# Optimization experiments

Hardware: AMD Instinct MI355X
Metric: run time of the kernel (lower is better)

Reference implementation:

```python
import jax, jax.numpy as jnp
import numpy as np
from jax.ops import segment_sum, segment_max

N, E, B, F, CG = 20000, 320000, 64, 256, 92
NL, NP = 4, 3  # transformer conv layers, ppe layers
SQ = float(np.sqrt(F))


def setup_inputs() -> dict:
    ks = iter(jax.random.split(jax.random.key(0), 64))
    p = lambda *s: jax.random.normal(next(ks), s, jnp.float32) * 0.02
    return {
        "x": jax.random.uniform(next(ks), (N, CG), jnp.float32, 0.0, 10.0),
        "edge_index": jax.random.randint(next(ks), (2, E), 0, N, dtype=jnp.int32),
        "edge_attr": jax.random.normal(next(ks), (E, 3), jnp.float32),
        "batch": jnp.sort(jax.random.randint(next(ks), (N,), 0, B, dtype=jnp.int32)),
        "num_osda": jax.random.uniform(next(ks), (B,), jnp.float32, 1.0, 4.0),
        "ae_W1": p(F, CG), "ae_b1": p(F), "ae_W2": p(F, F), "ae_b2": p(F),
        "ee_W": p(F, F), "ee_b": p(F),
        "pe_W": p(F, CG), "pe_b": p(F),
        "Wq": p(NL, F, F), "bq": p(NL, F), "Wk": p(NL, F, F), "bk": p(NL, F),
        "Wv": p(NL, F, F), "bv": p(NL, F), "We": p(NL, F, F), "be": p(NL, F),
        "Ws": p(NL, F, F), "bs": p(NL, F),
        "pW1": p(NP, 2 * F, F), "pb1": p(NP, 2 * F),
        "pW2": p(NP, F, F), "pb2": p(NP, F),
        "pW3": p(NP, F, F), "pb3": p(NP, F),
        "pg": jnp.ones((NP, F), jnp.float32), "pbeta": jnp.zeros((NP, F), jnp.float32),
        "fc_W": p(F, F), "fc_b": p(F), "out_W": p(1, F), "out_b": p(1),
    }


def _forward(x, edge_index, edge_attr, batch, num_osda, ae_W1, ae_b1, ae_W2, ae_b2,
             ee_W, ee_b, pe_W, pe_b, Wq, bq, Wk, bk, Wv, bv, We, be, Ws, bs,
             pW1, pb1, pW2, pb2, pW3, pb3, pg, pbeta, fc_W, fc_b, out_W, out_b):
    src, dst = edge_index[0], edge_index[1]
    # atom embedding on floor(x): Lin -> SiLU -> Lin
    h = jax.nn.silu(jnp.floor(x) @ ae_W1.T + ae_b1) @ ae_W2.T + ae_b2   # [N,F]
    # ppe embedding on frac(x)*1000
    ppe = ((x - jnp.trunc(x)) * 1000.0) @ pe_W.T + pe_b                 # [N,F]
    # edge embedding: scalar -1/||edge_attr|| -> RBF(vmin=-6,vmax=0,bins=256) -> Lin -> SiLU
    d = -1.0 / jnp.linalg.norm(edge_attr, axis=1)                       # [E]
    centers = jnp.linspace(-6.0, 0.0, F)
    gamma = 1.0 / (6.0 / (F - 1))  # 1/mean(diff(centers))
    rbf = jnp.exp(-gamma * (d[:, None] - centers) ** 2)                 # [E,F]
    ef = jax.nn.silu(rbf @ ee_W.T + ee_b)                               # [E,F]

    def conv(h, i):
        # graph transformer conv (heads=1): softmax over incoming edges per node
        q = h @ Wq[i].T + bq[i]
        k = h @ Wk[i].T + bk[i]
        v = h @ Wv[i].T + bv[i]
        e = ef @ We[i].T + be[i]
        kj = k[src] + e                                                 # [E,F]
        vj = v[src] + e                                                 # [E,F]
        s = jnp.sum(q[dst] * kj, axis=-1) / SQ                          # [E]
        m = segment_max(s, dst, num_segments=N)
        ex = jnp.exp(s - m[dst])
        den = segment_sum(ex, dst, num_segments=N)
        alpha = ex / den[dst]
        agg = segment_sum(alpha[:, None] * vj, dst, num_segments=N)     # [N,F]
        return agg + h @ Ws[i].T + bs[i]                                # root/skip

    def ppe_conv(h, adj, i):
        adj = adj + h
        bn = adj * pg[i] + pbeta[i]  # eval-mode BatchNorm1d (running mean 0, var 1)
        a2 = bn @ pW1[i].T + pb1[i]                                     # [N,2F]
        x1 = a2[:, :F] @ pW2[i].T + pb2[i]
        x2 = jax.nn.gelu(a2[:, F:], approximate=False)  # dropout = identity (eval)
        return (x1 * x2) @ pW3[i].T + pb3[i] + h, adj

    for i in range(NP):
        h = conv(h, i)
        h, ppe = ppe_conv(h, ppe, i)
    h = conv(h, NL - 1)

    # scatter-mean pooling over graphs
    cnt = jnp.maximum(segment_sum(jnp.ones((N,), h.dtype), batch, num_segments=B), 1.0)
    tot = segment_sum(h, batch, num_segments=B) / cnt[:, None]          # [B,F]
    crystal = tot + jax.nn.silu(tot @ fc_W.T + fc_b)
    out = crystal @ out_W.T + out_b                                     # [B,1]
    return jnp.squeeze(out, -1) / num_osda                             # [B]


def reference(x, edge_index, edge_attr, batch, num_osda, ae_W1, ae_b1, ae_W2, ae_b2,
              ee_W, ee_b, pe_W, pe_b, Wq, bq, Wk, bk, Wv, bv, We, be, Ws, bs,
              pW1, pb1, pW2, pb2, pW3, pb3, pg, pbeta, fc_W, fc_b, out_W, out_b):
    return _forward(x, edge_index, edge_attr, batch, num_osda, ae_W1, ae_b1, ae_W2, ae_b2,
                    ee_W, ee_b, pe_W, pe_b, Wq, bq, Wk, bk, Wv, bv, We, be, Ws, bs,
                    pW1, pb1, pW2, pb2, pW3, pb3, pg, pbeta, fc_W, fc_b, out_W, out_b)
```

## Files before the change

### kernel.cpp

```cpp
#include <hip/hip_runtime.h>
#include <cstdint>
#include <cstddef>


#define DEVFN static __device__ __forceinline__

DEVFN float siluf(float x) { return x / (1.f + expf(-x)); }

DEVFN unsigned short f2bf(float x) {
    union { float f; unsigned u; } v; v.f = x;
    return (unsigned short)((v.u + 0x7FFFu + ((v.u >> 16) & 1u)) >> 16);
}
DEVFN float bf2f(unsigned short h) {
    union { unsigned u; float f; } v; v.u = ((unsigned)h) << 16;
    return v.f;
}

typedef __attribute__((ext_vector_type(8))) short bf16x8;
typedef __attribute__((ext_vector_type(4))) float f32x4;

#define O_F32    0
#define O_F32P   1
#define O_PPE1   4
#define O_PLANES 5

template <int ACT, int OMODE>
__launch_bounds__(256) __global__
void gemm_spp(const short* __restrict__ Ahi, const short* __restrict__ Alo, int lda,
              const short* __restrict__ Whi, const short* __restrict__ Wlo, int ldw,
              const float* __restrict__ bias,
              const float* __restrict__ res, int ldr,
              float* __restrict__ C, short* __restrict__ P1, short* __restrict__ P2,
              int ldc, int M, int OUT, int K)
{
    constexpr int LDP = 40;
    __shared__ short AsH[128 * LDP];
    __shared__ short AsL[128 * LDP];
    __shared__ short WsH[128 * LDP];
    __shared__ short WsL[128 * LDP];
    const int tid = threadIdx.x;
    const int bm = blockIdx.x * 128;
    const int bn = blockIdx.y * 128;
    const int w = tid >> 6, lane = tid & 63;
    const int wm = (w >> 1) * 64, wn = (w & 1) * 64;
    const int lr = lane & 15, lc = lane >> 4;

    f32x4 acc[4][4];
#pragma unroll
    for (int i = 0; i < 4; ++i)
#pragma unroll
        for (int j = 0; j < 4; ++j) acc[i][j] = (f32x4){0.f, 0.f, 0.f, 0.f};

    const int srow = tid & 127;
    const int scol0 = (tid >> 7) * 16;

    for (int k0 = 0; k0 < K; k0 += 32) {
        {
            int gm = bm + srow;
            if (gm < M) {
                const short* ah = Ahi + (size_t)gm * lda + k0 + scol0;
                const short* al = Alo + (size_t)gm * lda + k0 + scol0;
                *reinterpret_cast<bf16x8*>(&AsH[srow * LDP + scol0])     = *reinterpret_cast<const bf16x8*>(ah);
                *reinterpret_cast<bf16x8*>(&AsH[srow * LDP + scol0 + 8]) = *reinterpret_cast<const bf16x8*>(ah + 8);
                *reinterpret_cast<bf16x8*>(&AsL[srow * LDP + scol0])     = *reinterpret_cast<const bf16x8*>(al);
                *reinterpret_cast<bf16x8*>(&AsL[srow * LDP + scol0 + 8]) = *reinterpret_cast<const bf16x8*>(al + 8);
            } else {
                bf16x8 z = {0, 0, 0, 0, 0, 0, 0, 0};
                *reinterpret_cast<bf16x8*>(&AsH[srow * LDP + scol0])     = z;
                *reinterpret_cast<bf16x8*>(&AsH[srow * LDP + scol0 + 8]) = z;
                *reinterpret_cast<bf16x8*>(&AsL[srow * LDP + scol0])     = z;
                *reinterpret_cast<bf16x8*>(&AsL[srow * LDP + scol0 + 8]) = z;
            }
        }
        {
            int go = bn + srow;
            if (go < OUT) {
                const short* wh = Whi + (size_t)go * ldw + k0 + scol0;
                const short* wl = Wlo + (size_t)go * ldw + k0 + scol0;
                *reinterpret_cast<bf16x8*>(&WsH[srow * LDP + scol0])     = *reinterpret_cast<const bf16x8*>(wh);
                *reinterpret_cast<bf16x8*>(&WsH[srow * LDP + scol0 + 8]) = *reinterpret_cast<const bf16x8*>(wh + 8);
                *reinterpret_cast<bf16x8*>(&WsL[srow * LDP + scol0])     = *reinterpret_cast<const bf16x8*>(wl);
                *reinterpret_cast<bf16x8*>(&WsL[srow * LDP + scol0 + 8]) = *reinterpret_cast<const bf16x8*>(wl + 8);
            } else {
                bf16x8 z = {0, 0, 0, 0, 0, 0, 0, 0};
                *reinterpret_cast<bf16x8*>(&WsH[srow * LDP + scol0])     = z;
                *reinterpret_cast<bf16x8*>(&WsH[srow * LDP + scol0 + 8]) = z;
                *reinterpret_cast<bf16x8*>(&WsL[srow * LDP + scol0])     = z;
                *reinterpret_cast<bf16x8*>(&WsL[srow * LDP + scol0 + 8]) = z;
            }
        }
        __syncthreads();

        bf16x8 afh[4], afl[4], bfh[4], bfl[4];
#pragma unroll
        for (int f = 0; f < 4; ++f) {
            afh[f] = *reinterpret_cast<const bf16x8*>(&AsH[(wm + f * 16 + lr) * LDP + lc * 8]);
            afl[f] = *reinterpret_cast<const bf16x8*>(&AsL[(wm + f * 16 + lr) * LDP + lc * 8]);
            bfh[f] = *reinterpret_cast<const bf16x8*>(&WsH[(wn + f * 16 + lr) * LDP + lc * 8]);
            bfl[f] = *reinterpret_cast<const bf16x8*>(&WsL[(wn + f * 16 + lr) * LDP + lc * 8]);
        }
#pragma unroll
        for (int i = 0; i < 4; ++i)
#pragma unroll
            for (int j = 0; j < 4; ++j) {
                acc[i][j] = __builtin_amdgcn_mfma_f32_16x16x32_bf16(afh[i], bfh[j], acc[i][j], 0, 0, 0);
                acc[i][j] = __builtin_amdgcn_mfma_f32_16x16x32_bf16(afh[i], bfl[j], acc[i][j], 0, 0, 0);
                acc[i][j] = __builtin_amdgcn_mfma_f32_16x16x32_bf16(afl[i], bfh[j], acc[i][j], 0, 0, 0);
            }
        __syncthreads();
    }

#pragma unroll
    for (int i = 0; i < 4; ++i) {
#pragma unroll
        for (int j = 0; j < 4; ++j) {
            int col = bn + wn + j * 16 + lr;
            if (col >= OUT) continue;
            float bv = bias ? bias[col] : 0.f;
#pragma unroll
            for (int r = 0; r < 4; ++r) {
                int m = bm + wm + i * 16 + lc * 4 + r;
                if (m >= M) continue;
                float v = acc[i][j][r] + bv;
                if (ACT == 1) v = siluf(v);
                if (OMODE == O_F32) {
                    if (res) v += res[(size_t)m * ldr + col];
                    C[(size_t)m * ldc + col] = v;
                } else if (OMODE == O_F32P) {
                    if (res) v += res[(size_t)m * ldr + col];
                    C[(size_t)m * ldc + col] = v;
                    unsigned short hi = f2bf(v);
                    P1[(size_t)m * ldc + col] = (short)hi;
                    P2[(size_t)m * ldc + col] = (short)f2bf(v - bf2f(hi));
                } else if (OMODE == O_PPE1) {
                    if (col < 256) {
                        unsigned short hi = f2bf(v);
                        P1[(size_t)m * 256 + col] = (short)hi;
                        P2[(size_t)m * 256 + col] = (short)f2bf(v - bf2f(hi));
                    } else {
                        C[(size_t)m * 256 + (col - 256)] = v;
                    }
                } else {
                    unsigned short hi = f2bf(v);
                    P1[(size_t)m * ldc + col] = (short)hi;
                    P2[(size_t)m * ldc + col] = (short)f2bf(v - bf2f(hi));
                }
            }
        }
    }
}

template <int BM, int BN, int TM, int TN, int ACT>
__launch_bounds__(256) __global__
void gemm_nt(const float* __restrict__ A, int lda,
             const float* __restrict__ W,
             const float* __restrict__ bias,
             const float* __restrict__ res, int ldr,
             float* __restrict__ C, int ldc,
             int M, int K, int OUT)
{
    constexpr int BK = 16;
    __shared__ alignas(16) float As[BK][BM];
    __shared__ alignas(16) float Bs[BK][BN];
    const int tid = threadIdx.x;
    const int bm = blockIdx.x * BM;
    const int bn = blockIdx.y * BN;
    const int tr = (tid >> 4) * TM;
    const int tc = (tid & 15) * TN;

    float acc[TM][TN];
#pragma unroll
    for (int i = 0; i < TM; ++i)
#pragma unroll
        for (int j = 0; j < TN; ++j) acc[i][j] = 0.f;

    for (int k0 = 0; k0 < K; k0 += BK) {
#pragma unroll
        for (int it = 0; it < BM / 64; ++it) {
            int idx = tid + it * 256;
            int m = idx >> 2, kq = idx & 3;
            int gm = bm + m, gk = k0 + kq * 4;
            float t[4] = {0.f, 0.f, 0.f, 0.f};
            if (gm < M) {
#pragma unroll
                for (int j = 0; j < 4; ++j)
                    if (gk + j < K) t[j] = A[(size_t)gm * lda + gk + j];
            }
            As[kq * 4 + 0][m] = t[0];
            As[kq * 4 + 1][m] = t[1];
            As[kq * 4 + 2][m] = t[2];
            As[kq * 4 + 3][m] = t[3];
        }
#pragma unroll
        for (int it = 0; it < BN / 64; ++it) {
            int idx = tid + it * 256;
            int o = idx >> 2, kq = idx & 3;
            int go = bn + o, gk = k0 + kq * 4;
            float t[4] = {0.f, 0.f, 0.f, 0.f};
            if (go < OUT) {
#pragma unroll
                for (int j = 0; j < 4; ++j)
                    if (gk + j < K) t[j] = W[(size_t)go * K + gk + j];
            }
            Bs[kq * 4 + 0][o] = t[0];
            Bs[kq * 4 + 1][o] = t[1];
            Bs[kq * 4 + 2][o] = t[2];
            Bs[kq * 4 + 3][o] = t[3];
        }
        __syncthreads();
#pragma unroll
        for (int kk = 0; kk < BK; ++kk) {
            float a[TM], b[TN];
#pragma unroll
            for (int p = 0; p < TM; ++p) a[p] = As[kk][tr + p];
#pragma unroll
            for (int p = 0; p < TN; ++p) b[p] = Bs[kk][tc + p];
#pragma unroll
            for (int i = 0; i < TM; ++i)
#pragma unroll
                for (int j = 0; j < TN; ++j) acc[i][j] += a[i] * b[j];
        }
        __syncthreads();
    }

#pragma unroll
    for (int i = 0; i < TM; ++i) {
        int m = bm + tr + i;
        if (m >= M) continue;
#pragma unroll
        for (int j = 0; j < TN; ++j) {
            int o = bn + tc + j;
            if (o >= OUT) continue;
            float v = acc[i][j];
            if (bias) v += bias[o];
            if (ACT == 1) v = siluf(v);
            if (res) v += res[(size_t)m * ldr + o];
            C[(size_t)m * ldc + o] = v;
        }
    }
}

__global__ void split_w_k(const float* __restrict__ src, short* __restrict__ dhi,
                          short* __restrict__ dlo, int OUT, int K, int Kp)
{
    int idx = blockIdx.x * blockDim.x + threadIdx.x;
    if (idx >= OUT * Kp) return;
    int row = idx / Kp, col = idx - row * Kp;
    float v = (col < K) ? src[(size_t)row * K + col] : 0.f;
    unsigned short hi = f2bf(v);
    dhi[idx] = (short)hi;
    dlo[idx] = (short)f2bf(v - bf2f(hi));
}

__global__ void stack_qkvs_w_k(const float* __restrict__ Wq, const float* __restrict__ Wk,
                               const float* __restrict__ Wv, const float* __restrict__ Ws,
                               short* __restrict__ dhi, short* __restrict__ dlo, int total)
{
    int idx = blockIdx.x * blockDim.x + threadIdx.x;
    if (idx >= total) return;
    int col = idx & 255;
    int row = (idx >> 8) & 1023;
    int layer = idx >> 18;
    int s2 = row >> 8;
    const float* s = (s2 == 0) ? Wq : ((s2 == 1) ? Wk : ((s2 == 2) ? Wv : Ws));
    float v = s[(size_t)layer * 65536 + (size_t)(row & 255) * 256 + col];
    unsigned short hi = f2bf(v);
    dhi[idx] = (short)hi;
    dlo[idx] = (short)f2bf(v - bf2f(hi));
}

__global__ void stack_qkvs_b_k(const float* __restrict__ bq, const float* __restrict__ bk,
                               const float* __restrict__ bv, const float* __restrict__ bs,
                               float* __restrict__ dst, int total)
{
    int idx = blockIdx.x * blockDim.x + threadIdx.x;
    if (idx >= total) return;
    int r = idx & 1023, layer = idx >> 10;
    int s2 = r >> 8;
    const float* s = (s2 == 0) ? bq : ((s2 == 1) ? bk : ((s2 == 2) ? bv : bs));
    dst[idx] = s[layer * 256 + (r & 255)];
}

__global__ void node_prep_k(const float* __restrict__ x,
                            short* __restrict__ fxHi, short* __restrict__ fxLo,
                            short* __restrict__ pxHi, short* __restrict__ pxLo, int n96)
{
    int idx = blockIdx.x * blockDim.x + threadIdx.x;
    if (idx >= n96) return;
    int n = idx / 96, c = idx - n * 96;
    float fv = 0.f, pv = 0.f;
    if (c < 92) {
        float v = x[(size_t)n * 92 + c];
        fv = floorf(v);
        pv = (v - truncf(v)) * 1000.f;
    }
    unsigned short h1 = f2bf(fv);
    fxHi[idx] = (short)h1; fxLo[idx] = (short)f2bf(fv - bf2f(h1));
    unsigned short h2 = f2bf(pv);
    pxHi[idx] = (short)h2; pxLo[idx] = (short)f2bf(pv - bf2f(h2));
}

__global__ void table_rbf_k(short* __restrict__ dhi, short* __restrict__ dlo,
                            int T, float dmin, float step)
{
    int idx = blockIdx.x * blockDim.x + threadIdx.x;
    if (idx >= T * 64) return;
    int t = idx >> 6, j4 = (idx & 63) * 4;
    float dv = dmin + step * (float)t;
    short h4[4], l4[4];
#pragma unroll
    for (int j = 0; j < 4; ++j) {
        float c = -6.f + 6.f * (float)(j4 + j) * (1.f / 255.f);
        float u = dv - c;
        float r = expf(-42.5f * u * u);
        unsigned short hi = f2bf(r);
        h4[j] = (short)hi;
        l4[j] = (short)f2bf(r - bf2f(hi));
    }
    *reinterpret_cast<short4*>(dhi + (size_t)t * 256 + j4) = *reinterpret_cast<short4*>(h4);
    *reinterpret_cast<short4*>(dlo + (size_t)t * 256 + j4) = *reinterpret_cast<short4*>(l4);
}

__global__ void edge_prep_k(const float* __restrict__ ea, int* __restrict__ i0,
                            float* __restrict__ fr, int E, float dmin, float invstep, int T)
{
    int i = blockIdx.x * blockDim.x + threadIdx.x;
    if (i < E) {
        float a = ea[(size_t)i * 3], b = ea[(size_t)i * 3 + 1], c = ea[(size_t)i * 3 + 2];
        float d = -1.f / sqrtf(a * a + b * b + c * c);
        float u = (d - dmin) * invstep;
        u = fminf(fmaxf(u, 0.f), (float)(T - 1) - 1e-3f);
        int t0 = (int)u;
        i0[i] = t0;
        fr[i] = u - (float)t0;
    }
}

__global__ void ppe_prep_k(float* __restrict__ ppe, const float* __restrict__ h,
                           const float* __restrict__ pg, const float* __restrict__ pbeta,
                           short* __restrict__ s1Hi, short* __restrict__ s1Lo, int n)
{
    int i = blockIdx.x * blockDim.x + threadIdx.x;
    if (i < n) {
        float adj = ppe[i] + h[i];
        ppe[i] = adj;
        int f = i & 255;
        float bn = adj * pg[f] + pbeta[f];
        unsigned short hi = f2bf(bn);
        s1Hi[i] = (short)hi;
        s1Lo[i] = (short)f2bf(bn - bf2f(hi));
    }
}

__global__ void gate_k(const float* __restrict__ x1, const float* __restrict__ x2b,
                       short* __restrict__ s3Hi, short* __restrict__ s3Lo, int n)
{
    int i = blockIdx.x * blockDim.x + threadIdx.x;
    if (i < n) {
        float x2 = x2b[i];
        float ge = 0.5f * x2 * (1.f + erff(x2 * 0.70710678118654752f));
        float g = x1[i] * ge;
        unsigned short hi = f2bf(g);
        s3Hi[i] = (short)hi;
        s3Lo[i] = (short)f2bf(g - bf2f(hi));
    }
}

__global__ void hist_k(const int* __restrict__ dst, int* __restrict__ deg, int E)
{
    int i = blockIdx.x * blockDim.x + threadIdx.x;
    if (i < E) atomicAdd(&deg[dst[i]], 1);
}

__global__ void scan_k(const int* __restrict__ deg, int* __restrict__ off, int n)
{
    __shared__ int buf[1024];
    __shared__ int carry;
    const int t = threadIdx.x;
    if (t == 0) carry = 0;
    __syncthreads();
    for (int base = 0; base < n; base += 1024) {
        int i = base + t;
        int v = (i < n) ? deg[i] : 0;
        buf[t] = v;
        __syncthreads();
        for (int s = 1; s < 1024; s <<= 1) {
            int add = (t >= s) ? buf[t - s] : 0;
            __syncthreads();
            buf[t] += add;
            __syncthreads();
        }
        if (i < n) off[i] = carry + buf[t] - v;
        __syncthreads();
        if (t == 0) carry += buf[1023];
        __syncthreads();
    }
    if (t == 0) off[n] = carry;
}

__global__ void copy_int_k(const int* __restrict__ a, int* __restrict__ b, int n)
{
    int i = blockIdx.x * blockDim.x + threadIdx.x;
    if (i < n) b[i] = a[i];
}

__global__ void scatter_k(const int* __restrict__ dst, int* __restrict__ cursor,
                          int* __restrict__ esort, int E)
{
    int i = blockIdx.x * blockDim.x + threadIdx.x;
    if (i < E) {
        int p = atomicAdd(&cursor[dst[i]], 1);
        esort[p] = i;
    }
}

__launch_bounds__(256) __global__
void attn_fused_k(const float* __restrict__ qkvs, const float* __restrict__ etab,
                  const int* __restrict__ ei0, const float* __restrict__ efr,
                  const int* __restrict__ src, const int* __restrict__ esort,
                  const int* __restrict__ off, float* __restrict__ hn, int Nn)
{
    int node = blockIdx.x * 4 + (threadIdx.x >> 6);
    if (node >= Nn) return;
    int lane = threadIdx.x & 63;
    int lo = off[node], hi = off[node + 1];

    const float* qrow = qkvs + (size_t)node * 1024;
    float4 qv = *reinterpret_cast<const float4*>(qrow + lane * 4);
    float4 sk = *reinterpret_cast<const float4*>(qrow + 768 + lane * 4);

    float m = -3.4e38f, den = 0.f;
    float ax = 0.f, ay = 0.f, az = 0.f, aw = 0.f;

    for (int jj = lo; jj < hi; ++jj) {
        int eid = esort[jj];
        int sp = src[eid];
        int t0 = ei0[eid];
        float f = efr[eid];
        const float* srow = qkvs + (size_t)sp * 1024;
        float4 kv = *reinterpret_cast<const float4*>(srow + 256 + lane * 4);
        float4 e0 = *reinterpret_cast<const float4*>(etab + (size_t)t0 * 256 + lane * 4);
        float4 e1 = *reinterpret_cast<const float4*>(etab + (size_t)(t0 + 1) * 256 + lane * 4);
        float ex0 = e0.x + f * (e1.x - e0.x);
        float ex1 = e0.y + f * (e1.y - e0.y);
        float ex2 = e0.z + f * (e1.z - e0.z);
        float ex3 = e0.w + f * (e1.w - e0.w);
        float p = qv.x * (kv.x + ex0) + qv.y * (kv.y + ex1) +
                  qv.z * (kv.z + ex2) + qv.w * (kv.w + ex3);
#pragma unroll
        for (int s = 32; s; s >>= 1) p += __shfl_xor(p, s, 64);
        p *= 0.0625f;
        float4 vv = *reinterpret_cast<const float4*>(srow + 512 + lane * 4);
        float vx0 = vv.x + ex0, vx1 = vv.y + ex1, vx2 = vv.z + ex2, vx3 = vv.w + ex3;
        if (p > m) {
            float sc = expf(m - p);
            den = den * sc + 1.f;
            ax = ax * sc + vx0;
            ay = ay * sc + vx1;
            az = az * sc + vx2;
            aw = aw * sc + vx3;
            m = p;
        } else {
            float wgt = expf(p - m);
            den += wgt;
            ax += wgt * vx0;
            ay += wgt * vx1;
            az += wgt * vx2;
            aw += wgt * vx3;
        }
    }
    float inv = (hi > lo) ? 1.f / den : 0.f;
    float4 o = {sk.x + ax * inv, sk.y + ay * inv, sk.z + az * inv, sk.w + aw * inv};
    *reinterpret_cast<float4*>(hn + (size_t)node * 256 + lane * 4) = o;
}

__launch_bounds__(256) __global__
void pool_mean_k(const float* __restrict__ h, const int* __restrict__ batch,
                 float* __restrict__ tot, int Nn)
{
    int g = blockIdx.x;
    __shared__ int sl, sh;
    if (threadIdx.x == 0) {
        int lo = 0, hi = Nn;
        while (lo < hi) { int mid = (lo + hi) >> 1; if (batch[mid] < g) lo = mid + 1; else hi = mid; }
        sl = lo;
        lo = 0; hi = Nn;
        while (lo < hi) { int mid = (lo + hi) >> 1; if (batch[mid] < g + 1) lo = mid + 1; else hi = mid; }
        sh = lo;
    }
    __syncthreads();
    float acc = 0.f;
    for (int n = sl; n < sh; ++n) acc += h[(size_t)n * 256 + threadIdx.x];
    float c = (float)(sh - sl);
    if (c < 1.f) c = 1.f;
    tot[(size_t)g * 256 + threadIdx.x] = acc / c;
}

__launch_bounds__(256) __global__
void out_k(const float* __restrict__ crystal, const float* __restrict__ oW,
           const float* __restrict__ ob, const float* __restrict__ nosda,
           float* __restrict__ out, int Bn)
{
    int b = blockIdx.x;
    __shared__ float red[256];
    float p = crystal[(size_t)b * 256 + threadIdx.x] * oW[threadIdx.x];
    red[threadIdx.x] = p;
    __syncthreads();
    for (int s = 128; s; s >>= 1) {
        if (threadIdx.x < s) red[threadIdx.x] += red[threadIdx.x + s];
        __syncthreads();
    }
    if (threadIdx.x == 0) out[b] = (red[0] + ob[0]) / nosda[b];
}

extern "C" void kernel_launch(void* const* d_in, const int* in_sizes, int n_in,
                              void* d_out, int out_size, void* d_ws, size_t ws_size,
                              hipStream_t stream)
{
    const float* x     = (const float*)d_in[0];
    const int*   ei    = (const int*)d_in[1];
    const float* ea    = (const float*)d_in[2];
    const int*   batch = (const int*)d_in[3];
    const float* nosda = (const float*)d_in[4];
    const float* ae_W1 = (const float*)d_in[5];
    const float* ae_b1 = (const float*)d_in[6];
    const float* ae_W2 = (const float*)d_in[7];
    const float* ae_b2 = (const float*)d_in[8];
    const float* ee_W  = (const float*)d_in[9];
    const float* ee_b  = (const float*)d_in[10];
    const float* pe_W  = (const float*)d_in[11];
    const float* pe_b  = (const float*)d_in[12];
    const float* Wq    = (const float*)d_in[13];
    const float* bq    = (const float*)d_in[14];
    const float* Wk    = (const float*)d_in[15];
    const float* bk    = (const float*)d_in[16];
    const float* Wv    = (const float*)d_in[17];
    const float* bv    = (const float*)d_in[18];
    const float* We    = (const float*)d_in[19];
    const float* be    = (const float*)d_in[20];
    const float* Ws    = (const float*)d_in[21];
    const float* bs    = (const float*)d_in[22];
    const float* pW1   = (const float*)d_in[23];
    const float* pb1   = (const float*)d_in[24];
    const float* pW2   = (const float*)d_in[25];
    const float* pb2   = (const float*)d_in[26];
    const float* pW3   = (const float*)d_in[27];
    const float* pb3   = (const float*)d_in[28];
    const float* pg    = (const float*)d_in[29];
    const float* pbeta = (const float*)d_in[30];
    const float* fc_W  = (const float*)d_in[31];
    const float* fc_b  = (const float*)d_in[32];
    const float* out_W = (const float*)d_in[33];
    const float* out_b = (const float*)d_in[34];

    const int CG = 92, F = 256;
    const int N = in_sizes[0] / CG;
    const int E = in_sizes[1] / 2;
    const int B = in_sizes[4];
    const int T = 4096;
    const float DMIN = -8.f, DMAX = 0.f;
    const float STEP = (DMAX - DMIN) / (float)(T - 1);
    const int* src  = ei;
    const int* dstp = ei + E;

    float* w = (float*)d_ws;
    auto take = [&](size_t n) { float* p = w; w += n; return p; };
    auto takeS = [&](size_t nshorts) { short* p = (short*)w; w += (nshorts + 1) / 2; return p; };
    const size_t NF = (size_t)N * F;
    float* hb0  = take(NF);
    float* hb1  = take(NF);
    float* ppeb = take(NF);
    short* hHi  = takeS(NF);
    short* hLo  = takeS(NF);
    short* s1Hi = takeS(NF);
    short* s1Lo = takeS(NF);
    float* etab = take((size_t)4 * T * F);
    float* arena = take((size_t)N * 1024);
    float* efr  = take(E);
    float* totb = take((size_t)B * F);
    float* cryb = take((size_t)B * F);
    float* bstk = take(4 * 1024);
    short* qwHi = takeS((size_t)4 * 1024 * 256);
    short* qwLo = takeS((size_t)4 * 1024 * 256);
    short* eeHi = takeS((size_t)256 * 256);
    short* eeLo = takeS((size_t)256 * 256);
    short* weHi = takeS((size_t)4 * 256 * 256);
    short* weLo = takeS((size_t)4 * 256 * 256);
    short* a1Hi = takeS((size_t)256 * 96);
    short* a1Lo = takeS((size_t)256 * 96);
    short* a2Hi = takeS((size_t)256 * 256);
    short* a2Lo = takeS((size_t)256 * 256);
    short* peHi = takeS((size_t)256 * 96);
    short* peLo = takeS((size_t)256 * 96);
    short* p1Hi = takeS((size_t)3 * 512 * 256);
    short* p1Lo = takeS((size_t)3 * 512 * 256);
    short* p2Hi = takeS((size_t)3 * 256 * 256);
    short* p2Lo = takeS((size_t)3 * 256 * 256);
    short* p3Hi = takeS((size_t)3 * 256 * 256);
    short* p3Lo = takeS((size_t)3 * 256 * 256);
    int* ei0    = (int*)w; w += E;
    int* deg    = (int*)w; w += N;
    int* offb   = (int*)w; w += (N + 1);
    int* curb   = (int*)w; w += N;
    int* esort  = (int*)w; w += E;
    size_t need = (size_t)((char*)w - (char*)d_ws);
    if (need > ws_size) return;
    (void)n_in; (void)out_size;

    short* fxHi = (short*)arena;
    short* fxLo = fxHi + (size_t)N * 96;
    short* pxHi = fxLo + (size_t)N * 96;
    short* pxLo = pxHi + (size_t)N * 96;
    short* rbHi = pxLo + (size_t)N * 96;
    short* rbLo = rbHi + (size_t)T * 256;
    short* efHi = rbLo + (size_t)T * 256;
    short* efLo = efHi + (size_t)T * 256;
    short* embHi = efLo + (size_t)T * 256;
    short* embLo = embHi + NF;
    float* qkvs = arena;
    short* a2b1Hi = (short*)arena;
    short* a2b1Lo = a2b1Hi + NF;
    float* x2b = arena + NF;
    float* s2b = x2b + NF;
    short* s3Hi = (short*)(s2b + NF);
    short* s3Lo = s3Hi + NF;

    dim3 blk(256);
    auto g1 = [](int n) { return dim3((n + 255) / 256); };

    node_prep_k<<<g1(N * 96), blk, 0, stream>>>(x, fxHi, fxLo, pxHi, pxLo, N * 96);
    edge_prep_k<<<g1(E), blk, 0, stream>>>(ea, ei0, efr, E, DMIN, 1.f / STEP, T);
    table_rbf_k<<<g1(T * 64), blk, 0, stream>>>(rbHi, rbLo, T, DMIN, STEP);

    stack_qkvs_w_k<<<g1(4 * 1024 * 256), blk, 0, stream>>>(Wq, Wk, Wv, Ws, qwHi, qwLo, 4 * 1024 * 256);
    stack_qkvs_b_k<<<g1(4 * 1024), blk, 0, stream>>>(bq, bk, bv, bs, bstk, 4 * 1024);
    split_w_k<<<g1(256 * 256), blk, 0, stream>>>(ee_W, eeHi, eeLo, 256, 256, 256);
    split_w_k<<<g1(4 * 256 * 256), blk, 0, stream>>>(We, weHi, weLo, 1024, 256, 256);
    split_w_k<<<g1(256 * 96), blk, 0, stream>>>(ae_W1, a1Hi, a1Lo, 256, 92, 96);
    split_w_k<<<g1(256 * 256), blk, 0, stream>>>(ae_W2, a2Hi, a2Lo, 256, 256, 256);
    split_w_k<<<g1(256 * 96), blk, 0, stream>>>(pe_W, peHi, peLo, 256, 92, 96);
    split_w_k<<<g1(3 * 512 * 256), blk, 0, stream>>>(pW1, p1Hi, p1Lo, 1536, 256, 256);
    split_w_k<<<g1(3 * 256 * 256), blk, 0, stream>>>(pW2, p2Hi, p2Lo, 768, 256, 256);
    split_w_k<<<g1(3 * 256 * 256), blk, 0, stream>>>(pW3, p3Hi, p3Lo, 768, 256, 256);

    {
        dim3 grid((T + 127) / 128, 2);
        gemm_spp<1, O_PLANES><<<grid, blk, 0, stream>>>(rbHi, rbLo, 256, eeHi, eeLo, 256,
                                                        ee_b, nullptr, 0, nullptr, efHi, efLo, 256, T, 256, 256);
        for (int i = 0; i < 4; ++i)
            gemm_spp<0, O_F32><<<grid, blk, 0, stream>>>(efHi, efLo, 256,
                weHi + (size_t)i * 65536, weLo + (size_t)i * 65536, 256,
                be + (size_t)i * F, nullptr, 0, etab + (size_t)i * T * F, nullptr, nullptr, 256, T, 256, 256);
    }

    {
        dim3 grid((N + 127) / 128, 2);
        gemm_spp<1, O_PLANES><<<grid, blk, 0, stream>>>(fxHi, fxLo, 96, a1Hi, a1Lo, 96,
                                                        ae_b1, nullptr, 0, nullptr, embHi, embLo, 256, N, 256, 96);
        gemm_spp<0, O_F32P><<<grid, blk, 0, stream>>>(embHi, embLo, 256, a2Hi, a2Lo, 256,
                                                      ae_b2, nullptr, 0, hb0, hHi, hLo, 256, N, 256, 256);
        gemm_spp<0, O_F32><<<grid, blk, 0, stream>>>(pxHi, pxLo, 96, peHi, peLo, 96,
                                                     pe_b, nullptr, 0, ppeb, nullptr, nullptr, 256, N, 256, 96);
    }

    hipMemsetAsync(deg, 0, (size_t)N * sizeof(int), stream);
    hist_k<<<g1(E), blk, 0, stream>>>(dstp, deg, E);
    scan_k<<<1, 1024, 0, stream>>>(deg, offb, N);
    copy_int_k<<<g1(N), blk, 0, stream>>>(offb, curb, N);
    scatter_k<<<g1(E), blk, 0, stream>>>(dstp, curb, esort, E);

    float* h  = hb0;
    float* hn = hb1;
    for (int i = 0; i < 4; ++i) {
        {
            dim3 grid((N + 127) / 128, 8);
            gemm_spp<0, O_F32><<<grid, blk, 0, stream>>>(hHi, hLo, 256,
                qwHi + (size_t)i * 262144, qwLo + (size_t)i * 262144, 256,
                bstk + (size_t)i * 1024, nullptr, 0, qkvs, nullptr, nullptr, 1024, N, 1024, 256);
        }

        attn_fused_k<<<dim3((N + 3) / 4), blk, 0, stream>>>(
            qkvs, etab + (size_t)i * T * F, ei0, efr, src, esort, offb, hn, N);
        { float* t = h; h = hn; hn = t; }

        if (i < 3) {
            ppe_prep_k<<<g1(N * F), blk, 0, stream>>>(ppeb, h, pg + (size_t)i * F, pbeta + (size_t)i * F,
                                                      s1Hi, s1Lo, N * F);
            {
                dim3 grid((N + 127) / 128, 4);
                gemm_spp<0, O_PPE1><<<grid, blk, 0, stream>>>(s1Hi, s1Lo, 256,
                    p1Hi + (size_t)i * 131072, p1Lo + (size_t)i * 131072, 256,
                    pb1 + (size_t)i * 512, nullptr, 0, x2b, a2b1Hi, a2b1Lo, 0, N, 512, 256);
            }
            {
                dim3 grid((N + 127) / 128, 2);
                gemm_spp<0, O_F32><<<grid, blk, 0, stream>>>(a2b1Hi, a2b1Lo, 256,
                    p2Hi + (size_t)i * 65536, p2Lo + (size_t)i * 65536, 256,
                    pb2 + (size_t)i * F, nullptr, 0, s2b, nullptr, nullptr, 256, N, 256, 256);
            }
            gate_k<<<g1(N * F), blk, 0, stream>>>(s2b, x2b, s3Hi, s3Lo, N * F);
            {
                dim3 grid((N + 127) / 128, 2);
                gemm_spp<0, O_F32P><<<grid, blk, 0, stream>>>(s3Hi, s3Lo, 256,
                    p3Hi + (size_t)i * 65536, p3Lo + (size_t)i * 65536, 256,
                    pb3 + (size_t)i * F, h, 256, hn, hHi, hLo, 256, N, 256, 256);
            }
            { float* t = h; h = hn; hn = t; }
        }
    }

    pool_mean_k<<<dim3(B), blk, 0, stream>>>(h, batch, totb, N);
    {
        dim3 grid((B + 63) / 64, (F + 63) / 64);
        gemm_nt<64, 64, 4, 4, 1><<<grid, blk, 0, stream>>>(totb, F, fc_W, fc_b, totb, F, cryb, F, B, F, F);
    }
    out_k<<<dim3(B), blk, 0, stream>>>(cryb, out_W, out_b, nosda, (float*)d_out, B);
}
```

Before: 1.858 ms.

## Fuse ppe prep into attention, gate into GEMM epilogue, batch edge-table GEMMs

Folds the ppe residual-add, affine normalisation and bf16 split-plane conversion into the attention kernel's epilogue, and moves the GELU gating into a new GEMM output mode. This removes two elementwise kernels and their full N×F round trips through memory. The four per-layer edge-table GEMMs become one wider GEMM with a strided table layout (ldt=1024). The attention loop now processes two edges per iteration with two independent online-softmax accumulators that are merged at the end, which raises memory-level parallelism at the cost of more registers.

```diff
diff --git a/kernel.cpp b/kernel.cpp
--- a/kernel.cpp
+++ b/kernel.cpp
@@ -23,6 +23,7 @@
 #define O_F32P   1
 #define O_PPE1   4
 #define O_PLANES 5
+#define O_GATE   6
 
 template <int ACT, int OMODE>
 __launch_bounds__(256) __global__
@@ -140,6 +141,13 @@
                     } else {
                         C[(size_t)m * 256 + (col - 256)] = v;
                     }
+                } else if (OMODE == O_GATE) {
+                    float x2 = res[(size_t)m * ldr + col];
+                    float ge = 0.5f * x2 * (1.f + erff(x2 * 0.70710678118654752f));
+                    float g = v * ge;
+                    unsigned short hi = f2bf(g);
+                    P1[(size_t)m * ldc + col] = (short)hi;
+                    P2[(size_t)m * ldc + col] = (short)f2bf(g - bf2f(hi));
                 } else {
                     unsigned short hi = f2bf(v);
                     P1[(size_t)m * ldc + col] = (short)hi;
@@ -333,36 +341,6 @@
         int t0 = (int)u;
         i0[i] = t0;
         fr[i] = u - (float)t0;
-    }
-}
-
-__global__ void ppe_prep_k(float* __restrict__ ppe, const float* __restrict__ h,
-                           const float* __restrict__ pg, const float* __restrict__ pbeta,
-                           short* __restrict__ s1Hi, short* __restrict__ s1Lo, int n)
-{
-    int i = blockIdx.x * blockDim.x + threadIdx.x;
-    if (i < n) {
-        float adj = ppe[i] + h[i];
-        ppe[i] = adj;
-        int f = i & 255;
-        float bn = adj * pg[f] + pbeta[f];
-        unsigned short hi = f2bf(bn);
-        s1Hi[i] = (short)hi;
-        s1Lo[i] = (short)f2bf(bn - bf2f(hi));
-    }
-}
-
-__global__ void gate_k(const float* __restrict__ x1, const float* __restrict__ x2b,
-                       short* __restrict__ s3Hi, short* __restrict__ s3Lo, int n)
-{
-    int i = blockIdx.x * blockDim.x + threadIdx.x;
-    if (i < n) {
-        float x2 = x2b[i];
-        float ge = 0.5f * x2 * (1.f + erff(x2 * 0.70710678118654752f));
-        float g = x1[i] * ge;
-        unsigned short hi = f2bf(g);
-        s3Hi[i] = (short)hi;
-        s3Lo[i] = (short)f2bf(g - bf2f(hi));
     }
 }
 
@@ -415,10 +393,13 @@
 }
 
 __launch_bounds__(256) __global__
-void attn_fused_k(const float* __restrict__ qkvs, const float* __restrict__ etab,
+void attn_fused_k(const float* __restrict__ qkvs, const float* __restrict__ etab, int ldt,
                   const int* __restrict__ ei0, const float* __restrict__ efr,
                   const int* __restrict__ src, const int* __restrict__ esort,
-                  const int* __restrict__ off, float* __restrict__ hn, int Nn)
+                  const int* __restrict__ off, float* __restrict__ hn,
+                  float* __restrict__ ppeb, const float* __restrict__ pg,
+                  const float* __restrict__ pbeta,
+                  short* __restrict__ s1Hi, short* __restrict__ s1Lo, int Nn)
 {
     int node = blockIdx.x * 4 + (threadIdx.x >> 6);
     if (node >= Nn) return;
@@ -429,49 +410,104 @@
     float4 qv = *reinterpret_cast<const float4*>(qrow + lane * 4);
     float4 sk = *reinterpret_cast<const float4*>(qrow + 768 + lane * 4);
 
-    float m = -3.4e38f, den = 0.f;
-    float ax = 0.f, ay = 0.f, az = 0.f, aw = 0.f;
-
-    for (int jj = lo; jj < hi; ++jj) {
-        int eid = esort[jj];
-        int sp = src[eid];
-        int t0 = ei0[eid];
-        float f = efr[eid];
-        const float* srow = qkvs + (size_t)sp * 1024;
-        float4 kv = *reinterpret_cast<const float4*>(srow + 256 + lane * 4);
-        float4 e0 = *reinterpret_cast<const float4*>(etab + (size_t)t0 * 256 + lane * 4);
-        float4 e1 = *reinterpret_cast<const float4*>(etab + (size_t)(t0 + 1) * 256 + lane * 4);
-        float ex0 = e0.x + f * (e1.x - e0.x);
-        float ex1 = e0.y + f * (e1.y - e0.y);
-        float ex2 = e0.z + f * (e1.z - e0.z);
-        float ex3 = e0.w + f * (e1.w - e0.w);
-        float p = qv.x * (kv.x + ex0) + qv.y * (kv.y + ex1) +
-                  qv.z * (kv.z + ex2) + qv.w * (kv.w + ex3);
-#pragma unroll
-        for (int s = 32; s; s >>= 1) p += __shfl_xor(p, s, 64);
-        p *= 0.0625f;
-        float4 vv = *reinterpret_cast<const float4*>(srow + 512 + lane * 4);
-        float vx0 = vv.x + ex0, vx1 = vv.y + ex1, vx2 = vv.z + ex2, vx3 = vv.w + ex3;
-        if (p > m) {
-            float sc = expf(m - p);
-            den = den * sc + 1.f;
-            ax = ax * sc + vx0;
-            ay = ay * sc + vx1;
-            az = az * sc + vx2;
-            aw = aw * sc + vx3;
-            m = p;
+    float m0 = -3.4e38f, d0 = 0.f, x0 = 0.f, y0 = 0.f, z0 = 0.f, w0 = 0.f;
+    float m1 = -3.4e38f, d1 = 0.f, x1 = 0.f, y1 = 0.f, z1 = 0.f, w1 = 0.f;
+
+    for (int jj = lo; jj < hi; jj += 2) {
+        bool hasB = (jj + 1 < hi);
+        int eidA = esort[jj];
+        int eidB = esort[hasB ? jj + 1 : jj];
+        int spA = src[eidA], spB = src[eidB];
+        int tA = ei0[eidA], tB = ei0[eidB];
+        float fA = efr[eidA], fB = efr[eidB];
+        const float* rA = qkvs + (size_t)spA * 1024;
+        const float* rB = qkvs + (size_t)spB * 1024;
+        float4 kA = *reinterpret_cast<const float4*>(rA + 256 + lane * 4);
+        float4 vA = *reinterpret_cast<const float4*>(rA + 512 + lane * 4);
+        float4 eA0 = *reinterpret_cast<const float4*>(etab + (size_t)tA * ldt + lane * 4);
+        float4 eA1 = *reinterpret_cast<const float4*>(etab + (size_t)(tA + 1) * ldt + lane * 4);
+        float4 kB = *reinterpret_cast<const float4*>(rB + 256 + lane * 4);
+        float4 vB = *reinterpret_cast<const float4*>(rB + 512 + lane * 4);
+        float4 eB0 = *reinterpret_cast<const float4*>(etab + (size_t)tB * ldt + lane * 4);
+        float4 eB1 = *reinterpret_cast<const float4*>(etab + (size_t)(tB + 1) * ldt + lane * 4);
+
+        float exA0 = eA0.x + fA * (eA1.x - eA0.x);
+        float exA1 = eA0.y + fA * (eA1.y - eA0.y);
+        float exA2 = eA0.z + fA * (eA1.z - eA0.z);
+        float exA3 = eA0.w + fA * (eA1.w - eA0.w);
+        float exB0 = eB0.x + fB * (eB1.x - eB0.x);
+        float exB1 = eB0.y + fB * (eB1.y - eB0.y);
+        float exB2 = eB0.z + fB * (eB1.z - eB0.z);
+        float exB3 = eB0.w + fB * (eB1.w - eB0.w);
+
+        float pA = qv.x * (kA.x + exA0) + qv.y * (kA.y + exA1) +
+                   qv.z * (kA.z + exA2) + qv.w * (kA.w + exA3);
+        float pB = qv.x * (kB.x + exB0) + qv.y * (kB.y + exB1) +
+                   qv.z * (kB.z + exB2) + qv.w * (kB.w + exB3);
+#pragma unroll
+        for (int s = 32; s; s >>= 1) {
+            pA += __shfl_xor(pA, s, 64);
+            pB += __shfl_xor(pB, s, 64);
+        }
+        pA *= 0.0625f;
+        pB *= 0.0625f;
+
+        float vxA0 = vA.x + exA0, vxA1 = vA.y + exA1, vxA2 = vA.z + exA2, vxA3 = vA.w + exA3;
+        if (pA > m0) {
+            float sc = expf(m0 - pA);
+            d0 = d0 * sc + 1.f;
+            x0 = x0 * sc + vxA0; y0 = y0 * sc + vxA1;
+            z0 = z0 * sc + vxA2; w0 = w0 * sc + vxA3;
+            m0 = pA;
         } else {
-            float wgt = expf(p - m);
-            den += wgt;
-            ax += wgt * vx0;
-            ay += wgt * vx1;
-            az += wgt * vx2;
-            aw += wgt * vx3;
-        }
-    }
+            float wg = expf(pA - m0);
+            d0 += wg;
+            x0 += wg * vxA0; y0 += wg * vxA1; z0 += wg * vxA2; w0 += wg * vxA3;
+        }
+        if (hasB) {
+            float vxB0 = vB.x + exB0, vxB1 = vB.y + exB1, vxB2 = vB.z + exB2, vxB3 = vB.w + exB3;
+            if (pB > m1) {
+                float sc = expf(m1 - pB);
+                d1 = d1 * sc + 1.f;
+                x1 = x1 * sc + vxB0; y1 = y1 * sc + vxB1;
+                z1 = z1 * sc + vxB2; w1 = w1 * sc + vxB3;
+                m1 = pB;
+            } else {
+                float wg = expf(pB - m1);
+                d1 += wg;
+                x1 += wg * vxB0; y1 += wg * vxB1; z1 += wg * vxB2; w1 += wg * vxB3;
+            }
+        }
+    }
+    float mm = fmaxf(m0, m1);
+    float sA = (d0 > 0.f) ? expf(m0 - mm) : 0.f;
+    float sB = (d1 > 0.f) ? expf(m1 - mm) : 0.f;
+    float den = d0 * sA + d1 * sB;
+    float ax = x0 * sA + x1 * sB;
+    float ay = y0 * sA + y1 * sB;
+    float az = z0 * sA + z1 * sB;
+    float aw = w0 * sA + w1 * sB;
     float inv = (hi > lo) ? 1.f / den : 0.f;
     float4 o = {sk.x + ax * inv, sk.y + ay * inv, sk.z + az * inv, sk.w + aw * inv};
     *reinterpret_cast<float4*>(hn + (size_t)node * 256 + lane * 4) = o;
+
+    if (ppeb) {
+        float4 pp = *reinterpret_cast<const float4*>(ppeb + (size_t)node * 256 + lane * 4);
+        float4 adj = {pp.x + o.x, pp.y + o.y, pp.z + o.z, pp.w + o.w};
+        *reinterpret_cast<float4*>(ppeb + (size_t)node * 256 + lane * 4) = adj;
+        float4 g4 = *reinterpret_cast<const float4*>(pg + lane * 4);
+        float4 b4 = *reinterpret_cast<const float4*>(pbeta + lane * 4);
+        float bn0 = adj.x * g4.x + b4.x;
+        float bn1 = adj.y * g4.y + b4.y;
+        float bn2 = adj.z * g4.z + b4.z;
+        float bn3 = adj.w * g4.w + b4.w;
+        unsigned short h0 = f2bf(bn0), h1 = f2bf(bn1), h2 = f2bf(bn2), h3 = f2bf(bn3);
+        short4 hs = {(short)h0, (short)h1, (short)h2, (short)h3};
+        short4 ls = {(short)f2bf(bn0 - bf2f(h0)), (short)f2bf(bn1 - bf2f(h1)),
+                     (short)f2bf(bn2 - bf2f(h2)), (short)f2bf(bn3 - bf2f(h3))};
+        *reinterpret_cast<short4*>(s1Hi + (size_t)node * 256 + lane * 4) = hs;
+        *reinterpret_cast<short4*>(s1Lo + (size_t)node * 256 + lane * 4) = ls;
+    }
 }
 
 __launch_bounds__(256) __global__
@@ -621,8 +657,7 @@
     short* a2b1Hi = (short*)arena;
     short* a2b1Lo = a2b1Hi + NF;
     float* x2b = arena + NF;
-    float* s2b = x2b + NF;
-    short* s3Hi = (short*)(s2b + NF);
+    short* s3Hi = (short*)(arena + 2 * NF);
     short* s3Lo = s3Hi + NF;
 
     dim3 blk(256);
@@ -647,10 +682,11 @@
         dim3 grid((T + 127) / 128, 2);
         gemm_spp<1, O_PLANES><<<grid, blk, 0, stream>>>(rbHi, rbLo, 256, eeHi, eeLo, 256,
                                                         ee_b, nullptr, 0, nullptr, efHi, efLo, 256, T, 256, 256);
-        for (int i = 0; i < 4; ++i)
-            gemm_spp<0, O_F32><<<grid, blk, 0, stream>>>(efHi, efLo, 256,
-                weHi + (size_t)i * 65536, weLo + (size_t)i * 65536, 256,
-                be + (size_t)i * F, nullptr, 0, etab + (size_t)i * T * F, nullptr, nullptr, 256, T, 256, 256);
+    }
+    {
+        dim3 grid((T + 127) / 128, 8);
+        gemm_spp<0, O_F32><<<grid, blk, 0, stream>>>(efHi, efLo, 256, weHi, weLo, 256,
+                                                     be, nullptr, 0, etab, nullptr, nullptr, 1024, T, 1024, 256);
     }
 
     {
@@ -679,13 +715,18 @@
                 bstk + (size_t)i * 1024, nullptr, 0, qkvs, nullptr, nullptr, 1024, N, 1024, 256);
         }
 
-        attn_fused_k<<<dim3((N + 3) / 4), blk, 0, stream>>>(
-            qkvs, etab + (size_t)i * T * F, ei0, efr, src, esort, offb, hn, N);
+        if (i < 3) {
+            attn_fused_k<<<dim3((N + 3) / 4), blk, 0, stream>>>(
+                qkvs, etab + (size_t)i * 256, 1024, ei0, efr, src, esort, offb, hn,
+                ppeb, pg + (size_t)i * F, pbeta + (size_t)i * F, s1Hi, s1Lo, N);
+        } else {
+            attn_fused_k<<<dim3((N + 3) / 4), blk, 0, stream>>>(
+                qkvs, etab + (size_t)i * 256, 1024, ei0, efr, src, esort, offb, hn,
+                nullptr, nullptr, nullptr, nullptr, nullptr, N);
+        }
         { float* t = h; h = hn; hn = t; }
 
         if (i < 3) {
-            ppe_prep_k<<<g1(N * F), blk, 0, stream>>>(ppeb, h, pg + (size_t)i * F, pbeta + (size_t)i * F,
-                                                      s1Hi, s1Lo, N * F);
             {
                 dim3 grid((N + 127) / 128, 4);
                 gemm_spp<0, O_PPE1><<<grid, blk, 0, stream>>>(s1Hi, s1Lo, 256,
@@ -694,11 +735,10 @@
             }
             {
                 dim3 grid((N + 127) / 128, 2);
-                gemm_spp<0, O_F32><<<grid, blk, 0, stream>>>(a2b1Hi, a2b1Lo, 256,
+                gemm_spp<0, O_GATE><<<grid, blk, 0, stream>>>(a2b1Hi, a2b1Lo, 256,
                     p2Hi + (size_t)i * 65536, p2Lo + (size_t)i * 65536, 256,
-                    pb2 + (size_t)i * F, nullptr, 0, s2b, nullptr, nullptr, 256, N, 256, 256);
-            }
-            gate_k<<<g1(N * F), blk, 0, stream>>>(s2b, x2b, s3Hi, s3Lo, N * F);
+                    pb2 + (size_t)i * F, x2b, 256, nullptr, s3Hi, s3Lo, 256, N, 256, 256);
+            }
             {
                 dim3 grid((N + 127) / 128, 2);
                 gemm_spp<0, O_F32P><<<grid, blk, 0, stream>>>(s3Hi, s3Lo, 256,
```

Result: faster. 1.775 ms (-4.4%).
